# Performance work log

Measured on AMD Instinct MI355X. Metric: run time of the kernel, lower is better.

## Reference

```python
import jax, jax.numpy as jnp
import numpy as np


def setup_inputs() -> dict:
    key = jax.random.key(0)
    ks = jax.random.split(key, 8)
    B, L, D = 8, 4096, 1024
    s = 1.0 / np.sqrt(D)  # torch Linear default init scale (approx)
    return {
        "x": jax.random.normal(ks[0], (B, L, D), dtype=jnp.float32),
        "hidden": jax.random.normal(ks[1], (B, D), dtype=jnp.float32),
        "W_f": jax.random.normal(ks[2], (D, D), dtype=jnp.float32) * s,
        "b_f": jnp.zeros((D,), dtype=jnp.float32),
        "W_i": jax.random.normal(ks[3], (D, D), dtype=jnp.float32) * s,
        "b_i": jnp.zeros((D,), dtype=jnp.float32),
        "W_o": jax.random.normal(ks[4], (D, D), dtype=jnp.float32) * s,
        "b_o": jnp.zeros((D,), dtype=jnp.float32),
    }


def reference(x, hidden, W_f, b_f, W_i, b_i, W_o, b_o):
    # x: [B, L, D], hidden: [B, D]
    D = x.shape[-1]
    lin = jnp.linspace(0.0, 1.0, D, dtype=x.dtype)  # per-channel gate scale
    remember = jax.nn.sigmoid(jnp.einsum('bld,ed->ble', x, W_f) + b_f) * lin
    forget = 1.0 - remember
    inp = jnp.tanh(jnp.einsum('bld,ed->ble', x, W_i) + b_i) * remember

    # linear recurrence h_t = forget_t * h_{t-1} + inp_t  via parallel scan
    def combine(c1, c2):
        a1, u1 = c1
        a2, u2 = c2
        return (a1 * a2, a2 * u1 + u2)

    cumprod_forget, h_inner = jax.lax.associative_scan(combine, (forget, inp), axis=1)
    h = h_inner + hidden[:, None, :] * cumprod_forget  # inject initial hidden state
    y = jnp.einsum('bld,ed->ble', h, W_o) + b_o
    return y, h
```

## Files before the change

### kernel.cpp

```cpp
#include <hip/hip_runtime.h>
#include <stdint.h>

#define B_ 8
#define L_ 4096
#define D_ 1024
#define M_ (B_*L_)
#define CHUNKS 128
#define TCH (L_/CHUNKS)

typedef float f32x4 __attribute__((ext_vector_type(4)));
typedef float f32x2 __attribute__((ext_vector_type(2)));
typedef short short8 __attribute__((ext_vector_type(8)));
typedef unsigned short ushort4v __attribute__((ext_vector_type(4)));

static __device__ __forceinline__ unsigned short f2bf(float f) {
  union { float f; unsigned u; } v; v.f = f;
  unsigned r = v.u + 0x7FFFu + ((v.u >> 16) & 1u);
  return (unsigned short)(r >> 16);
}
static __device__ __forceinline__ float bf2f(unsigned short u) {
  union { unsigned u; float f; } v; v.u = ((unsigned)u) << 16; return v.f;
}

#define GLOAD16(g, l) \
  __builtin_amdgcn_global_load_lds((__attribute__((address_space(1))) const void*)(g), \
                                   (__attribute__((address_space(3))) void*)(l), 16, 0, 0)

__global__ __launch_bounds__(256)
void cvt_all(const float* __restrict__ x,  const float* __restrict__ w0,
             const float* __restrict__ w1, const float* __restrict__ w2,
             unsigned short* __restrict__ dst)
{
  const int xn8 = (M_ * D_) / 8;
  const int wn8 = (D_ * D_) / 8;
  int gid = blockIdx.x * 256 + threadIdx.x;
  const float* src;
  size_t soff;
  if (gid < xn8)                { src = x;  soff = (size_t)gid * 8; }
  else if (gid < xn8 + wn8)     { src = w0; soff = (size_t)(gid - xn8) * 8; }
  else if (gid < xn8 + 2 * wn8) { src = w1; soff = (size_t)(gid - xn8 - wn8) * 8; }
  else                          { src = w2; soff = (size_t)(gid - xn8 - 2 * wn8) * 8; }
  const f32x4* s = (const f32x4*)(src + soff);
  f32x4 v0 = s[0], v1 = s[1];
  union { short8 v; unsigned short u[8]; } w;
  w.u[0] = f2bf(v0[0]); w.u[1] = f2bf(v0[1]); w.u[2] = f2bf(v0[2]); w.u[3] = f2bf(v0[3]);
  w.u[4] = f2bf(v1[0]); w.u[5] = f2bf(v1[1]); w.u[6] = f2bf(v1[2]); w.u[7] = f2bf(v1[3]);
  *(short8*)(dst + (size_t)gid * 8) = w.v;
}

template<int MODE>
__global__ __launch_bounds__(512, 2)
void gemm256(const unsigned short* __restrict__ A,
             const unsigned short* __restrict__ Bw,
             const float* __restrict__ bias0,
             const float* __restrict__ bias1,
             unsigned short* __restrict__ ob0,
             unsigned short* __restrict__ ob1,
             float* __restrict__ of)
{
  __shared__ unsigned short lds[81920];
  char* ldsb = (char*)lds;

  const int tid  = threadIdx.x;
  const int lane = tid & 63;
  const int wid  = tid >> 6;
  const int wm   = wid >> 2;
  const int wn   = wid & 3;
  const int frow = lane & 15, ks = lane >> 4;
  const int xsw  = (ks ^ ((frow >> 1) & 3)) << 4;

  constexpr int NBN = (MODE == 0) ? 8 : 4;
  constexpr int GBM = 32 / NBN;
  const int xcd   = blockIdx.x & 7;
  const int slot  = blockIdx.x >> 3;
  const int local = slot & 31;
  const int wrnd  = slot >> 5;
  const int bm = (xcd * 16 + wrnd * GBM + (local & (GBM - 1))) * 256;
  const int bn = (local / GBM) * 256;

  const int r0  = tid >> 2;
  const int scl = ((tid & 3) ^ ((r0 >> 1) & 3)) << 4;
  const char* pA = (const char*)A  + (size_t)(bm + r0) * 2048 + scl;
  const char* pB = (const char*)Bw + (size_t)(bn + r0) * 2048 + scl;
  const int dst16 = tid * 16;

  f32x4 acc[8][4] = {};
  short8 aq[4], bq[4];

  auto stgA = [&](int c, int sl) {
    const char* s = pA + c * 64;
    char* d = ldsb + sl * 16384 + dst16;
    GLOAD16(s,                      d);
    GLOAD16(s + (size_t)128 * 2048, d + 8192);
  };
  auto stgB = [&](int c, int sl) {
    const char* s = pB + c * 64;
    char* d = ldsb + 81920 + sl * 16384 + dst16;
    GLOAD16(s,                      d);
    GLOAD16(s + (size_t)128 * 2048, d + 8192);
  };
  auto ldAB4 = [&](const char* LA, const char* LB) {
    const char* ab = LA + (wm * 128 + frow) * 64 + xsw;
    const char* bb = LB + (wn * 64 + frow) * 64 + xsw;
    aq[0] = *(const short8*)(ab);
    bq[0] = *(const short8*)(bb);
    bq[1] = *(const short8*)(bb + 1024);
    bq[2] = *(const short8*)(bb + 2048);
    bq[3] = *(const short8*)(bb + 3072);
    aq[1] = *(const short8*)(ab + 1024);
    aq[2] = *(const short8*)(ab + 2048);
    aq[3] = *(const short8*)(ab + 3072);
  };
  auto ldA4 = [&](const char* LA) {
    const char* ab = LA + (wm * 128 + 64 + frow) * 64 + xsw;
    aq[0] = *(const short8*)(ab);
    aq[1] = *(const short8*)(ab + 1024);
    aq[2] = *(const short8*)(ab + 2048);
    aq[3] = *(const short8*)(ab + 3072);
  };
  auto mfma16 = [&](int ih) {
    #pragma unroll
    for (int i2 = 0; i2 < 4; ++i2) {
      #pragma unroll
      for (int j = 0; j < 4; ++j)
        acc[ih * 4 + i2][j] =
          __builtin_amdgcn_mfma_f32_16x16x32_bf16(aq[i2], bq[j], acc[ih * 4 + i2][j], 0, 0, 0);
    }
  };

#define BAR __builtin_amdgcn_s_barrier()
#define WAITV(N) asm volatile("s_waitcnt vmcnt(" #N ")" ::: "memory")
#define DO_CH(c, SL, SG, STG, WN)                                             \
  {                                                                           \
    const char* LA = ldsb + (SL) * 16384;                                     \
    const char* LB = ldsb + 81920 + (SL) * 16384;                             \
    ldAB4(LA, LB);                                                            \
    if (STG) stgA((c) + 4, (SG));                                             \
    mfma16(0);                                                                \
    ldA4(LA);                                                                 \
    if (STG) stgB((c) + 4, (SG));                                             \
    mfma16(1);                                                                \
    WAITV(WN);                                                                \
    BAR;                                                                      \
  }
#define DO_CH_LAST(SL)                                                        \
  {                                                                           \
    const char* LA = ldsb + (SL) * 16384;                                     \
    const char* LB = ldsb + 81920 + (SL) * 16384;                             \
    ldAB4(LA, LB);                                                            \
    mfma16(0);                                                                \
    ldA4(LA);                                                                 \
    mfma16(1);                                                                \
  }

  stgA(0, 0); stgB(0, 0);
  stgA(1, 1); stgB(1, 1);
  stgA(2, 2); stgB(2, 2);
  stgA(3, 3); stgB(3, 3);
  WAITV(12);
  BAR;

  DO_CH( 0, 0, 4, true, 12);
  DO_CH( 1, 1, 0, true, 12);
  DO_CH( 2, 2, 1, true, 12);
  DO_CH( 3, 3, 2, true, 12);
  DO_CH( 4, 4, 3, true, 12);
  DO_CH( 5, 0, 4, true, 12);
  DO_CH( 6, 1, 0, true, 12);
  DO_CH( 7, 2, 1, true, 12);
  DO_CH( 8, 3, 2, true, 12);
  DO_CH( 9, 4, 3, true, 12);
  DO_CH(10, 0, 4, true, 12);
  DO_CH(11, 1, 0, true, 12);
  DO_CH(12, 2, 1, true, 12);
  DO_CH(13, 3, 2, true, 12);
  DO_CH(14, 4, 3, true, 12);
  DO_CH(15, 0, 4, true, 12);
  DO_CH(16, 1, 0, true, 12);
  DO_CH(17, 2, 1, true, 12);
  DO_CH(18, 3, 2, true, 12);
  DO_CH(19, 4, 3, true, 12);
  DO_CH(20, 0, 4, true, 12);
  DO_CH(21, 1, 0, true, 12);
  DO_CH(22, 2, 1, true, 12);
  DO_CH(23, 3, 2, true, 12);
  DO_CH(24, 4, 3, true, 12);
  DO_CH(25, 0, 4, true, 12);
  DO_CH(26, 1, 0, true, 12);
  DO_CH(27, 2, 1, true, 12);
  DO_CH(28, 3, 0, false, 8);
  DO_CH(29, 4, 0, false, 4);
  DO_CH(30, 0, 0, false, 0);
  DO_CH_LAST(1);
#undef DO_CH
#undef DO_CH_LAST
#undef WAITV
#undef BAR

  if constexpr (MODE == 0) {
    const int plane = bn >> 10;
    const int cb    = bn & 1023;
    unsigned short* ob = plane ? ob1 : ob0;
    const float* bs    = plane ? bias1 : bias0;
    float bv[4];
    #pragma unroll
    for (int j = 0; j < 4; ++j) bv[j] = bs[cb + wn * 64 + j * 16 + frow];
    #pragma unroll
    for (int ii = 0; ii < 8; ++ii) {
      int row = bm + wm * 128 + ii * 16 + ks * 4;
      #pragma unroll
      for (int j = 0; j < 4; ++j) {
        int col = cb + wn * 64 + j * 16 + frow;
        float lin = (float)col * (1.0f / 1023.0f);
        #pragma unroll
        for (int r = 0; r < 4; ++r) {
          float z = acc[ii][j][r] + bv[j];
          float v;
          if (plane == 0) {
            v = lin / (1.0f + __expf(-z));
          } else {
            float e2 = __expf(2.0f * z);
            v = 1.0f - 2.0f / (e2 + 1.0f);
          }
          ob[(size_t)(row + r) * D_ + col] = f2bf(v);
        }
      }
    }
  } else {
    float bv[4];
    #pragma unroll
    for (int j = 0; j < 4; ++j) bv[j] = bias0[bn + wn * 64 + j * 16 + frow];
    #pragma unroll
    for (int ii = 0; ii < 8; ++ii) {
      int row = bm + wm * 128 + ii * 16 + ks * 4;
      #pragma unroll
      for (int j = 0; j < 4; ++j) {
        int col = bn + wn * 64 + j * 16 + frow;
        #pragma unroll
        for (int r = 0; r < 4; ++r)
          of[(size_t)(row + r) * D_ + col] = acc[ii][j][r] + bv[j];
      }
    }
  }
}

__global__ __launch_bounds__(256)
void scan_partial_b(const unsigned short* __restrict__ rb,
                    const unsigned short* __restrict__ tb,
                    float* __restrict__ Ag, float* __restrict__ Ug)
{
  int blk = blockIdx.x;
  int b = blk >> 7, c = blk & (CHUNKS - 1);
  int e = threadIdx.x << 2;
  size_t base = ((size_t)b * L_ + (size_t)c * TCH) * D_ + e;
  f32x4 a = {1.f,1.f,1.f,1.f}, u = {0.f,0.f,0.f,0.f};
  for (int t = 0; t < TCH; ++t) {
    ushort4v r4 = *(const ushort4v*)(rb + base + (size_t)t * D_);
    ushort4v t4 = *(const ushort4v*)(tb + base + (size_t)t * D_);
    #pragma unroll
    for (int j = 0; j < 4; ++j) {
      float rem = bf2f(r4[j]);
      float f   = 1.0f - rem;
      float inp = bf2f(t4[j]) * rem;
      u[j] = fmaf(f, u[j], inp);
      a[j] *= f;
    }
  }
  size_t o = (size_t)(b * CHUNKS + c) * D_ + e;
  *(f32x4*)(Ag + o) = a;
  *(f32x4*)(Ug + o) = u;
}

__global__ __launch_bounds__(256)
void scan_carry(const float* __restrict__ Ag, const float* __restrict__ Ug,
                const float* __restrict__ hidden, float* __restrict__ Hin)
{
  int gid = blockIdx.x * 256 + threadIdx.x;
  int b = gid >> 8;
  int e = (gid & 255) << 2;
  f32x4 h = *(const f32x4*)(hidden + (size_t)b * D_ + e);
  for (int c = 0; c < CHUNKS; ++c) {
    size_t o = (size_t)(b * CHUNKS + c) * D_ + e;
    *(f32x4*)(Hin + o) = h;
    f32x4 A = *(const f32x4*)(Ag + o);
    f32x4 U = *(const f32x4*)(Ug + o);
    h = A * h + U;
  }
}

__global__ __launch_bounds__(256)
void scan_apply_b(const unsigned short* __restrict__ rb,
                  const unsigned short* __restrict__ tb,
                  const float* __restrict__ Hin,
                  float* __restrict__ hout, unsigned short* __restrict__ hb)
{
  int blk = blockIdx.x;
  int b = blk >> 7, c = blk & (CHUNKS - 1);
  int e = threadIdx.x << 2;
  size_t base = ((size_t)b * L_ + (size_t)c * TCH) * D_ + e;
  f32x4 h = *(const f32x4*)(Hin + (size_t)(b * CHUNKS + c) * D_ + e);
  for (int t = 0; t < TCH; ++t) {
    size_t o = base + (size_t)t * D_;
    ushort4v r4 = *(const ushort4v*)(rb + o);
    ushort4v t4 = *(const ushort4v*)(tb + o);
    #pragma unroll
    for (int j = 0; j < 4; ++j) {
      float rem = bf2f(r4[j]);
      float f   = 1.0f - rem;
      float inp = bf2f(t4[j]) * rem;
      h[j] = fmaf(f, h[j], inp);
    }
    *(f32x4*)(hout + o) = h;
    ushort4v p;
    p[0] = f2bf(h[0]); p[1] = f2bf(h[1]); p[2] = f2bf(h[2]); p[3] = f2bf(h[3]);
    *(ushort4v*)(hb + o) = p;
  }
}

template<int MODE>
__global__ __launch_bounds__(256, 2)
void gemm_slow(const float* __restrict__ A, const float* __restrict__ B0,
               const float* __restrict__ B1, const float* __restrict__ bias0,
               const float* __restrict__ bias1, float* __restrict__ out0,
               float* __restrict__ out1)
{
  constexpr int BK = 32;
  __shared__ unsigned short As[128 * BK];
  __shared__ unsigned short Bs0[128 * BK];
  __shared__ unsigned short Bs1[(MODE == 0) ? (128 * BK) : 8];

  const int tid = threadIdx.x, lane = tid & 63, wave = tid >> 6;
  const int wr = wave >> 1, wc = wave & 1;
  const int bm = blockIdx.x * 128, bn = blockIdx.y * 128;
  f32x4 acc0[4][4] = {};
  f32x4 acc1[(MODE == 0) ? 4 : 1][(MODE == 0) ? 4 : 1] = {};
  const int frow = lane & 15, kslot = lane >> 4;
  const int xs = kslot ^ (frow & 3);

  auto stage = [&](const float* src, unsigned short* dst) {
    #pragma unroll
    for (int p = 0; p < 4; ++p) {
      int g = p * 256 + tid;
      int row = g >> 3, kq = (g & 7) << 2;
      f32x4 v = *(const f32x4*)(src + (size_t)row * D_ + kq);
      ushort4v w;
      w[0] = f2bf(v[0]); w[1] = f2bf(v[1]); w[2] = f2bf(v[2]); w[3] = f2bf(v[3]);
      int byte = kq << 1, slot = byte >> 4, sub = byte & 15;
      int off = row * 64 + ((slot ^ (row & 3)) << 4) + sub;
      *(ushort4v*)((char*)dst + off) = w;
    }
  };

  for (int k0 = 0; k0 < D_; k0 += BK) {
    stage(A + (size_t)bm * D_ + k0, As);
    stage(B0 + (size_t)bn * D_ + k0, Bs0);
    if constexpr (MODE == 0) stage(B1 + (size_t)bn * D_ + k0, Bs1);
    __syncthreads();
    short8 af[4], bf0[4], bf1[4];
    #pragma unroll
    for (int i = 0; i < 4; ++i) {
      int ar = wr * 64 + i * 16 + frow;
      af[i] = *(const short8*)((const char*)As + ar * 64 + (xs << 4));
      int br = wc * 64 + i * 16 + frow;
      bf0[i] = *(const short8*)((const char*)Bs0 + br * 64 + (xs << 4));
      if constexpr (MODE == 0)
        bf1[i] = *(const short8*)((const char*)Bs1 + br * 64 + (xs << 4));
    }
    #pragma unroll
    for (int i = 0; i < 4; ++i)
      #pragma unroll
      for (int j = 0; j < 4; ++j) {
        acc0[i][j] = __builtin_amdgcn_mfma_f32_16x16x32_bf16(af[i], bf0[j], acc0[i][j], 0, 0, 0);
        if constexpr (MODE == 0)
          acc1[i][j] = __builtin_amdgcn_mfma_f32_16x16x32_bf16(af[i], bf1[j], acc1[i][j], 0, 0, 0);
      }
    __syncthreads();
  }
  #pragma unroll
  for (int i = 0; i < 4; ++i)
    #pragma unroll
    for (int j = 0; j < 4; ++j)
      #pragma unroll
      for (int r = 0; r < 4; ++r) {
        int row = bm + wr * 64 + i * 16 + (lane >> 4) * 4 + r;
        int col = bn + wc * 64 + j * 16 + (lane & 15);
        size_t idx = (size_t)row * D_ + col;
        if constexpr (MODE == 0) {
          float zf = acc0[i][j][r] + bias0[col];
          float linv = (float)col * (1.0f / 1023.0f);
          float rem = linv / (1.0f + __expf(-zf));
          float zi = acc1[i][j][r] + bias1[col];
          float e2 = __expf(2.0f * zi);
          float th = 1.0f - 2.0f / (e2 + 1.0f);
          out0[idx] = 1.0f - rem;
          out1[idx] = th * rem;
        } else {
          out0[idx] = acc0[i][j][r] + bias0[col];
        }
      }
}

__global__ __launch_bounds__(256)
void scan_partial_f(const float* __restrict__ p0, const float* __restrict__ p1,
                    float* __restrict__ Ag, float* __restrict__ Ug)
{
  int blk = blockIdx.x;
  int b = blk / (CHUNKS * 2);
  int c = (blk >> 1) & (CHUNKS - 1);
  int e = ((blk & 1) << 9) + threadIdx.x * 2;
  size_t base = ((size_t)b * L_ + (size_t)c * TCH) * D_ + e;
  f32x2 a = {1.0f, 1.0f}, u = {0.0f, 0.0f};
  for (int t = 0; t < TCH; ++t) {
    f32x2 f = *(const f32x2*)(p0 + base + (size_t)t * D_);
    f32x2 i = *(const f32x2*)(p1 + base + (size_t)t * D_);
    u = f * u + i;
    a = a * f;
  }
  size_t o = (size_t)(b * CHUNKS + c) * D_ + e;
  *(f32x2*)(Ag + o) = a;
  *(f32x2*)(Ug + o) = u;
}

__global__ __launch_bounds__(256)
void scan_apply_f(const float* __restrict__ p0, float* __restrict__ p1_io,
                  const float* __restrict__ Hin)
{
  int blk = blockIdx.x;
  int b = blk / (CHUNKS * 2);
  int c = (blk >> 1) & (CHUNKS - 1);
  int e = ((blk & 1) << 9) + threadIdx.x * 2;
  size_t base = ((size_t)b * L_ + (size_t)c * TCH) * D_ + e;
  f32x2 h = *(const f32x2*)(Hin + (size_t)(b * CHUNKS + c) * D_ + e);
  for (int t = 0; t < TCH; ++t) {
    size_t o = base + (size_t)t * D_;
    f32x2 f = *(const f32x2*)(p0 + o);
    f32x2 i = *(const f32x2*)(p1_io + o);
    h = f * h + i;
    *(f32x2*)(p1_io + o) = h;
  }
}

extern "C" void kernel_launch(void* const* d_in, const int* in_sizes, int n_in,
                              void* d_out, int out_size, void* d_ws, size_t ws_size,
                              hipStream_t stream)
{
  const float* x      = (const float*)d_in[0];
  const float* hidden = (const float*)d_in[1];
  const float* W_f    = (const float*)d_in[2];
  const float* b_f    = (const float*)d_in[3];
  const float* W_i    = (const float*)d_in[4];
  const float* b_i    = (const float*)d_in[5];
  const float* W_o    = (const float*)d_in[6];
  const float* b_o    = (const float*)d_in[7];

  float* y = (float*)d_out;
  float* h = y + (size_t)M_ * D_;

  const size_t xb_elems = (size_t)M_ * D_;
  const size_t w_elems  = (size_t)D_ * D_;
  const size_t agg      = (size_t)B_ * CHUNKS * D_;
  const size_t need = (xb_elems * 3 + 3 * w_elems) * 2 + agg * 3 * 4;

  if (ws_size >= need) {
    unsigned short* xb  = (unsigned short*)d_ws;
    unsigned short* wfb = xb + xb_elems;
    unsigned short* wib = wfb + w_elems;
    unsigned short* wob = wib + w_elems;
    unsigned short* rbv = wob + w_elems;
    unsigned short* tbv = rbv + xb_elems;
    float* Ag  = (float*)(tbv + xb_elems);
    float* Ug  = Ag + agg;
    float* Hin = Ug + agg;

    int cblk = (int)((xb_elems + 3 * w_elems) / 8 / 256);
    cvt_all<<<cblk, 256, 0, stream>>>(x, W_f, W_i, W_o, xb);

    gemm256<0><<<1024, 512, 0, stream>>>(xb, wfb, b_f, b_i, rbv, tbv, nullptr);

    int pblocks = B_ * CHUNKS;
    scan_partial_b<<<pblocks, 256, 0, stream>>>(rbv, tbv, Ag, Ug);
    scan_carry<<<(B_ * D_ / 4) / 256, 256, 0, stream>>>(Ag, Ug, hidden, Hin);
    scan_apply_b<<<pblocks, 256, 0, stream>>>(rbv, tbv, Hin, h, xb);

    gemm256<1><<<512, 512, 0, stream>>>(xb, wob, b_o, nullptr, nullptr, nullptr, y);
  } else {
    float* Ag  = (float*)d_ws;
    float* Ug  = Ag + agg;
    float* Hin = Ug + agg;
    dim3 gg(M_ / 128, D_ / 128);
    int pblocks = B_ * CHUNKS * 2;

    gemm_slow<0><<<gg, 256, 0, stream>>>(x, W_f, W_i, b_f, b_i, y, h);
    scan_partial_f<<<pblocks, 256, 0, stream>>>(y, h, Ag, Ug);
    scan_carry<<<(B_ * D_ / 4) / 256, 256, 0, stream>>>(Ag, Ug, hidden, Hin);
    scan_apply_f<<<pblocks, 256, 0, stream>>>(y, h, Hin);
    gemm_slow<1><<<gg, 256, 0, stream>>>(h, W_o, nullptr, b_o, nullptr, y, nullptr);
  }
}
```

Baseline: 393.8 us.

## Shrink GEMM tile to 256x128 with triple-buffered A and double-buffered B

The bf16 MFMA GEMM moves from a 256x256 block tile with a 5-stage LDS ring to a 256x128 tile. A now uses 3 LDS stages and B uses 2, which cuts LDS from 160KB to 64KB and halves each wave's accumulators, with launch bounds raised to 4 blocks per CU. The aim is higher occupancy and more blocks, so that global-load latency is hidden by other blocks rather than by deep prefetch. In exchange, arithmetic intensity per block drops, the A tile is loaded twice as often overall, and the shallower pipeline may stall more.

```diff
diff --git a/kernel.cpp b/kernel.cpp
--- a/kernel.cpp
+++ b/kernel.cpp
@@ -49,8 +49,8 @@
 }
 
 template<int MODE>
-__global__ __launch_bounds__(512, 2)
-void gemm256(const unsigned short* __restrict__ A,
+__global__ __launch_bounds__(512, 4)
+void gemm128(const unsigned short* __restrict__ A,
              const unsigned short* __restrict__ Bw,
              const float* __restrict__ bias0,
              const float* __restrict__ bias1,
@@ -58,25 +58,25 @@
              unsigned short* __restrict__ ob1,
              float* __restrict__ of)
 {
-  __shared__ unsigned short lds[81920];
+  __shared__ unsigned short lds[32768];
   char* ldsb = (char*)lds;
 
   const int tid  = threadIdx.x;
   const int lane = tid & 63;
   const int wid  = tid >> 6;
-  const int wm   = wid >> 2;
-  const int wn   = wid & 3;
+  const int wm   = wid >> 1;
+  const int wn   = wid & 1;
   const int frow = lane & 15, ks = lane >> 4;
   const int xsw  = (ks ^ ((frow >> 1) & 3)) << 4;
 
-  constexpr int NBN = (MODE == 0) ? 8 : 4;
-  constexpr int GBM = 32 / NBN;
+  constexpr int NBN = (MODE == 0) ? 16 : 8;
+  constexpr int GBM = 64 / NBN;
   const int xcd   = blockIdx.x & 7;
   const int slot  = blockIdx.x >> 3;
-  const int local = slot & 31;
-  const int wrnd  = slot >> 5;
+  const int local = slot & 63;
+  const int wrnd  = slot >> 6;
   const int bm = (xcd * 16 + wrnd * GBM + (local & (GBM - 1))) * 256;
-  const int bn = (local / GBM) * 256;
+  const int bn = (local / GBM) * 128;
 
   const int r0  = tid >> 2;
   const int scl = ((tid & 3) ^ ((r0 >> 1) & 3)) << 4;
@@ -84,7 +84,7 @@
   const char* pB = (const char*)Bw + (size_t)(bn + r0) * 2048 + scl;
   const int dst16 = tid * 16;
 
-  f32x4 acc[8][4] = {};
+  f32x4 acc[4][4] = {};
   short8 aq[4], bq[4];
 
   auto stgA = [&](int c, int sl) {
@@ -95,12 +95,11 @@
   };
   auto stgB = [&](int c, int sl) {
     const char* s = pB + c * 64;
-    char* d = ldsb + 81920 + sl * 16384 + dst16;
-    GLOAD16(s,                      d);
-    GLOAD16(s + (size_t)128 * 2048, d + 8192);
+    char* d = ldsb + 49152 + sl * 8192 + dst16;
+    GLOAD16(s, d);
   };
-  auto ldAB4 = [&](const char* LA, const char* LB) {
-    const char* ab = LA + (wm * 128 + frow) * 64 + xsw;
+  auto ldAB = [&](const char* LA, const char* LB) {
+    const char* ab = LA + (wm * 64 + frow) * 64 + xsw;
     const char* bb = LB + (wn * 64 + frow) * 64 + xsw;
     aq[0] = *(const short8*)(ab);
     bq[0] = *(const short8*)(bb);
@@ -111,87 +110,73 @@
     aq[2] = *(const short8*)(ab + 2048);
     aq[3] = *(const short8*)(ab + 3072);
   };
-  auto ldA4 = [&](const char* LA) {
-    const char* ab = LA + (wm * 128 + 64 + frow) * 64 + xsw;
-    aq[0] = *(const short8*)(ab);
-    aq[1] = *(const short8*)(ab + 1024);
-    aq[2] = *(const short8*)(ab + 2048);
-    aq[3] = *(const short8*)(ab + 3072);
-  };
-  auto mfma16 = [&](int ih) {
-    #pragma unroll
-    for (int i2 = 0; i2 < 4; ++i2) {
+  auto mfma16 = [&]() {
+    #pragma unroll
+    for (int i = 0; i < 4; ++i)
       #pragma unroll
       for (int j = 0; j < 4; ++j)
-        acc[ih * 4 + i2][j] =
-          __builtin_amdgcn_mfma_f32_16x16x32_bf16(aq[i2], bq[j], acc[ih * 4 + i2][j], 0, 0, 0);
-    }
+        acc[i][j] = __builtin_amdgcn_mfma_f32_16x16x32_bf16(aq[i], bq[j], acc[i][j], 0, 0, 0);
   };
 
 #define BAR __builtin_amdgcn_s_barrier()
 #define WAITV(N) asm volatile("s_waitcnt vmcnt(" #N ")" ::: "memory")
-#define DO_CH(c, SL, SG, STG, WN)                                             \
+#define DO_CH(c, SA, SB, SGA, SGB, STGA, STGB, WN)                            \
   {                                                                           \
-    const char* LA = ldsb + (SL) * 16384;                                     \
-    const char* LB = ldsb + 81920 + (SL) * 16384;                             \
-    ldAB4(LA, LB);                                                            \
-    if (STG) stgA((c) + 4, (SG));                                             \
-    mfma16(0);                                                                \
-    ldA4(LA);                                                                 \
-    if (STG) stgB((c) + 4, (SG));                                             \
-    mfma16(1);                                                                \
+    const char* LA = ldsb + (SA) * 16384;                                     \
+    const char* LB = ldsb + 49152 + (SB) * 8192;                              \
+    ldAB(LA, LB);                                                             \
+    if (STGB) stgB((c) + 1, (SGB));                                           \
+    if (STGA) stgA((c) + 2, (SGA));                                           \
+    mfma16();                                                                 \
     WAITV(WN);                                                                \
     BAR;                                                                      \
   }
-#define DO_CH_LAST(SL)                                                        \
+#define DO_CH_LAST(SA, SB)                                                    \
   {                                                                           \
-    const char* LA = ldsb + (SL) * 16384;                                     \
-    const char* LB = ldsb + 81920 + (SL) * 16384;                             \
-    ldAB4(LA, LB);                                                            \
-    mfma16(0);                                                                \
-    ldA4(LA);                                                                 \
-    mfma16(1);                                                                \
-  }
-
-  stgA(0, 0); stgB(0, 0);
-  stgA(1, 1); stgB(1, 1);
-  stgA(2, 2); stgB(2, 2);
-  stgA(3, 3); stgB(3, 3);
-  WAITV(12);
+    const char* LA = ldsb + (SA) * 16384;                                     \
+    const char* LB = ldsb + 49152 + (SB) * 8192;                              \
+    ldAB(LA, LB);                                                             \
+    mfma16();                                                                 \
+  }
+
+  stgA(0, 0);
+  stgB(0, 0);
+  stgA(1, 1);
+  WAITV(2);
   BAR;
 
-  DO_CH( 0, 0, 4, true, 12);
-  DO_CH( 1, 1, 0, true, 12);
-  DO_CH( 2, 2, 1, true, 12);
-  DO_CH( 3, 3, 2, true, 12);
-  DO_CH( 4, 4, 3, true, 12);
-  DO_CH( 5, 0, 4, true, 12);
-  DO_CH( 6, 1, 0, true, 12);
-  DO_CH( 7, 2, 1, true, 12);
-  DO_CH( 8, 3, 2, true, 12);
-  DO_CH( 9, 4, 3, true, 12);
-  DO_CH(10, 0, 4, true, 12);
-  DO_CH(11, 1, 0, true, 12);
-  DO_CH(12, 2, 1, true, 12);
-  DO_CH(13, 3, 2, true, 12);
-  DO_CH(14, 4, 3, true, 12);
-  DO_CH(15, 0, 4, true, 12);
-  DO_CH(16, 1, 0, true, 12);
-  DO_CH(17, 2, 1, true, 12);
-  DO_CH(18, 3, 2, true, 12);
-  DO_CH(19, 4, 3, true, 12);
-  DO_CH(20, 0, 4, true, 12);
-  DO_CH(21, 1, 0, true, 12);
-  DO_CH(22, 2, 1, true, 12);
-  DO_CH(23, 3, 2, true, 12);
-  DO_CH(24, 4, 3, true, 12);
-  DO_CH(25, 0, 4, true, 12);
-  DO_CH(26, 1, 0, true, 12);
-  DO_CH(27, 2, 1, true, 12);
-  DO_CH(28, 3, 0, false, 8);
-  DO_CH(29, 4, 0, false, 4);
-  DO_CH(30, 0, 0, false, 0);
-  DO_CH_LAST(1);
+  DO_CH( 0, 0, 0, 2, 1, true, true, 2);
+  DO_CH( 1, 1, 1, 0, 0, true, true, 2);
+  DO_CH( 2, 2, 0, 1, 1, true, true, 2);
+  DO_CH( 3, 0, 1, 2, 0, true, true, 2);
+  DO_CH( 4, 1, 0, 0, 1, true, true, 2);
+  DO_CH( 5, 2, 1, 1, 0, true, true, 2);
+  DO_CH( 6, 0, 0, 2, 1, true, true, 2);
+  DO_CH( 7, 1, 1, 0, 0, true, true, 2);
+  DO_CH( 8, 2, 0, 1, 1, true, true, 2);
+  DO_CH( 9, 0, 1, 2, 0, true, true, 2);
+  DO_CH(10, 1, 0, 0, 1, true, true, 2);
+  DO_CH(11, 2, 1, 1, 0, true, true, 2);
+  DO_CH(12, 0, 0, 2, 1, true, true, 2);
+  DO_CH(13, 1, 1, 0, 0, true, true, 2);
+  DO_CH(14, 2, 0, 1, 1, true, true, 2);
+  DO_CH(15, 0, 1, 2, 0, true, true, 2);
+  DO_CH(16, 1, 0, 0, 1, true, true, 2);
+  DO_CH(17, 2, 1, 1, 0, true, true, 2);
+  DO_CH(18, 0, 0, 2, 1, true, true, 2);
+  DO_CH(19, 1, 1, 0, 0, true, true, 2);
+  DO_CH(20, 2, 0, 1, 1, true, true, 2);
+  DO_CH(21, 0, 1, 2, 0, true, true, 2);
+  DO_CH(22, 1, 0, 0, 1, true, true, 2);
+  DO_CH(23, 2, 1, 1, 0, true, true, 2);
+  DO_CH(24, 0, 0, 2, 1, true, true, 2);
+  DO_CH(25, 1, 1, 0, 0, true, true, 2);
+  DO_CH(26, 2, 0, 1, 1, true, true, 2);
+  DO_CH(27, 0, 1, 2, 0, true, true, 2);
+  DO_CH(28, 1, 0, 0, 1, true, true, 2);
+  DO_CH(29, 2, 1, 1, 0, true, true, 2);
+  DO_CH(30, 0, 0, 0, 1, false, true, 0);
+  DO_CH_LAST(1, 1);
 #undef DO_CH
 #undef DO_CH_LAST
 #undef WAITV
@@ -206,15 +191,15 @@
     #pragma unroll
     for (int j = 0; j < 4; ++j) bv[j] = bs[cb + wn * 64 + j * 16 + frow];
     #pragma unroll
-    for (int ii = 0; ii < 8; ++ii) {
-      int row = bm + wm * 128 + ii * 16 + ks * 4;
+    for (int i = 0; i < 4; ++i) {
+      int row = bm + wm * 64 + i * 16 + ks * 4;
       #pragma unroll
       for (int j = 0; j < 4; ++j) {
         int col = cb + wn * 64 + j * 16 + frow;
         float lin = (float)col * (1.0f / 1023.0f);
         #pragma unroll
         for (int r = 0; r < 4; ++r) {
-          float z = acc[ii][j][r] + bv[j];
+          float z = acc[i][j][r] + bv[j];
           float v;
           if (plane == 0) {
             v = lin / (1.0f + __expf(-z));
@@ -231,14 +216,14 @@
     #pragma unroll
     for (int j = 0; j < 4; ++j) bv[j] = bias0[bn + wn * 64 + j * 16 + frow];
     #pragma unroll
-    for (int ii = 0; ii < 8; ++ii) {
-      int row = bm + wm * 128 + ii * 16 + ks * 4;
+    for (int i = 0; i < 4; ++i) {
+      int row = bm + wm * 64 + i * 16 + ks * 4;
       #pragma unroll
       for (int j = 0; j < 4; ++j) {
         int col = bn + wn * 64 + j * 16 + frow;
         #pragma unroll
         for (int r = 0; r < 4; ++r)
-          of[(size_t)(row + r) * D_ + col] = acc[ii][j][r] + bv[j];
+          of[(size_t)(row + r) * D_ + col] = acc[i][j][r] + bv[j];
       }
     }
   }
@@ -475,14 +460,14 @@
     int cblk = (int)((xb_elems + 3 * w_elems) / 8 / 256);
     cvt_all<<<cblk, 256, 0, stream>>>(x, W_f, W_i, W_o, xb);
 
-    gemm256<0><<<1024, 512, 0, stream>>>(xb, wfb, b_f, b_i, rbv, tbv, nullptr);
+    gemm128<0><<<2048, 512, 0, stream>>>(xb, wfb, b_f, b_i, rbv, tbv, nullptr);
 
     int pblocks = B_ * CHUNKS;
     scan_partial_b<<<pblocks, 256, 0, stream>>>(rbv, tbv, Ag, Ug);
     scan_carry<<<(B_ * D_ / 4) / 256, 256, 0, stream>>>(Ag, Ug, hidden, Hin);
     scan_apply_b<<<pblocks, 256, 0, stream>>>(rbv, tbv, Hin, h, xb);
 
-    gemm256<1><<<512, 512, 0, stream>>>(xb, wob, b_o, nullptr, nullptr, nullptr, y);
+    gemm128<1><<<1024, 512, 0, stream>>>(xb, wob, b_o, nullptr, nullptr, nullptr, y);
   } else {
     float* Ag  = (float*)d_ws;
     float* Ug  = Ag + agg;
```

New measurement: 391.0 us. About the same (-0.7%).
